# Kernel tuning notes

Hardware: AMD Instinct MI355X
Metric: run time of the kernel (lower is better)

## Reference

```python
import jax, jax.numpy as jnp
import numpy as np

B, L, D, R = 8, 2048, 512, 512  # batch, seq, feature, n_rules


def setup_inputs() -> dict:
    key = jax.random.key(0)
    ks = jax.random.split(key, 6)
    query = jax.random.normal(ks[0], (B, L, D), dtype=jnp.float32)
    # to_q: Linear(D, D)
    Wq = jax.random.normal(ks[1], (D, D), dtype=jnp.float32) / np.sqrt(D)
    bq = jnp.zeros((D,), dtype=jnp.float32)
    # to_c: Linear(L, R)
    Wc = jax.random.normal(ks[2], (R, L), dtype=jnp.float32) / np.sqrt(L)
    bc = jnp.zeros((R,), dtype=jnp.float32)
    # fuzzy rule params, torch.rand init (uniform [0,1)); widths kept away from 0
    centers = jax.random.uniform(ks[3], (R, D), dtype=jnp.float32)
    widths = jax.random.uniform(ks[4], (R, D), dtype=jnp.float32, minval=0.1, maxval=1.0)
    return {"query": query, "Wq": Wq, "bq": bq, "Wc": Wc, "bc": bc,
            "centers": centers, "widths": widths}


def reference(query, Wq, bq, Wc, bc, centers, widths):
    # q = to_q(query)  (projection=True)
    q = query @ Wq.T + bq  # (B, L, D)
    # z[b,l,r] = -0.5 * mean_d (|q - c| / w)^2 ; abs is a no-op under the square,
    # so expand (q - c)^2 / w^2 into three GEMM-friendly terms (exact same math).
    inv_w2 = 1.0 / (widths * widths)                      # (R, D)
    qq = (q * q) @ inv_w2.T                               # (B, L, R)
    qc = q @ (centers * inv_w2).T                         # (B, L, R)
    cc = jnp.sum(centers * centers * inv_w2, axis=-1)     # (R,)
    z = -(0.5 / D) * (qq - 2.0 * qc + cc)                 # (B, L, R)
    Fss = jax.nn.softmax(z, axis=-1)                      # (B, L, R); dropout p=0
    # conq = to_c applied along the L axis of query, yielding (B, R, D)
    conq = jnp.einsum('bld,rl->brd', query, Wc) + bc[None, :, None]
    return Fss @ conq                                     # (B, L, D)
```

## Files before the change

kernel.cpp:

```cpp
#include <hip/hip_runtime.h>
#include <hip/hip_bf16.h>

constexpr int Bb = 8, Ls = 2048, Dd = 512, Rr = 512;
constexpr int M1 = Bb * Ls;

typedef _Float16 h8v __attribute__((ext_vector_type(8)));
typedef _Float16 h4v __attribute__((ext_vector_type(4)));
typedef float f4v __attribute__((ext_vector_type(4)));

__device__ __forceinline__ void async_copy16(const void* g, void* l) {
  __builtin_amdgcn_global_load_lds((const __attribute__((address_space(1))) unsigned int*)g,
                                   (__attribute__((address_space(3))) unsigned int*)l, 16, 0, 0);
}

__device__ __forceinline__ void swizzle_xy(int& x, int& yy) {
  const int NX = gridDim.x;
  const int lin = ((int)blockIdx.z * (int)gridDim.y + (int)blockIdx.y) * NX + (int)blockIdx.x;
  const int xcd = lin & 7;
  const int w = lin >> 3;
  x = w % NX;
  yy = (w / NX) * 8 + xcd;
}

__global__ __launch_bounds__(256) void prep_all(
    const float* __restrict__ q, _Float16* __restrict__ qs, _Float16* __restrict__ qt,
    const float* __restrict__ Wq, _Float16* __restrict__ wq,
    const float* __restrict__ Wc, _Float16* __restrict__ wc,
    const float* __restrict__ centers, const float* __restrict__ widths,
    _Float16* __restrict__ iwh, _Float16* __restrict__ c2h, float* __restrict__ cc) {
  const int bid = blockIdx.x, tid = threadIdx.x;
  if (bid < 2048) {
    __shared__ float t[64][65];
    const int b = bid >> 8;
    const int l0 = ((bid >> 3) & 31) * 64;
    const int d0 = (bid & 7) * 64;
    const int r = tid >> 4, c4 = (tid & 15) * 4;
#pragma unroll
    for (int i = 0; i < 4; ++i) {
      const int l = r + i * 16;
      const float4 v = *(const float4*)&q[((long)b * Ls + l0 + l) * Dd + d0 + c4];
      t[l][c4] = v.x; t[l][c4 + 1] = v.y; t[l][c4 + 2] = v.z; t[l][c4 + 3] = v.w;
      h4v h = {(_Float16)v.x, (_Float16)v.y, (_Float16)v.z, (_Float16)v.w};
      *(h4v*)&qs[((long)b * Ls + l0 + l) * Dd + d0 + c4] = h;
    }
    __syncthreads();
#pragma unroll
    for (int i = 0; i < 4; ++i) {
      const int d = r + i * 16;
      h4v h = {(_Float16)t[c4][d], (_Float16)t[c4 + 1][d],
               (_Float16)t[c4 + 2][d], (_Float16)t[c4 + 3][d]};
      *(h4v*)&qt[((long)b * Dd + d0 + d) * Ls + l0 + c4] = h;
    }
  } else if (bid < 2304) {
    const int i = (bid - 2048) * 256 + tid;
    float4 v = *(const float4*)&Wq[(long)i * 4];
    h4v o = {(_Float16)v.x, (_Float16)v.y, (_Float16)v.z, (_Float16)v.w};
    *(h4v*)&wq[(long)i * 4] = o;
  } else if (bid < 3328) {
    const int i = (bid - 2304) * 256 + tid;
    float4 v = *(const float4*)&Wc[(long)i * 4];
    h4v o = {(_Float16)v.x, (_Float16)v.y, (_Float16)v.z, (_Float16)v.w};
    *(h4v*)&wc[(long)i * 4] = o;
  } else {
    const int wave = tid >> 6, lane = tid & 63;
    const int r = (bid - 3328) * 4 + wave;
    float s = 0.f;
#pragma unroll
    for (int j = 0; j < 8; ++j) {
      const int d = j * 64 + lane;
      const float c = centers[(long)r * Dd + d];
      const float w = widths[(long)r * Dd + d];
      const float iw = 1.0f / (w * w);
      iwh[(long)r * Dd + d] = (_Float16)iw;
      c2h[(long)r * Dd + d] = (_Float16)(-2.0f * c * iw);
      s += c * c * iw;
    }
#pragma unroll
    for (int o = 32; o > 0; o >>= 1) s += __shfl_xor(s, o, 64);
    if (lane == 0) cc[r] = s;
  }
}

template <int WM, int EPI>
__global__ __launch_bounds__(512, 4) void gemm_h(
    const _Float16* __restrict__ A, const _Float16* __restrict__ Bm,
    const float* __restrict__ bias, float* __restrict__ Cf,
    _Float16* __restrict__ Ch, int Kext, int ldA, int ldB, int ldC, int kstep,
    long sA, long sB, long sC) {
  constexpr int TM = WM * 32;
  __shared__ _Float16 As[2][TM * 32];
  __shared__ _Float16 Bs[2][128 * 32];
  int x, yy;
  swizzle_xy(x, yy);
  const int y = yy % (int)gridDim.y;
  const int zz = yy / (int)gridDim.y;
  const int n0 = x * 128;
  const int m0 = y * TM;
  const int kb = zz * kstep;
  const _Float16* Ab = A + (long)zz * sA;
  const _Float16* Bb = Bm + (long)zz * sB;

  const int tid = threadIdx.x;
  const int wave = tid >> 6, lane = tid & 63;
  const int wm = wave >> 2, wn = wave & 3;
  const int quad = lane >> 4, tr = lane & 15;
  const int lrow = lane >> 2;
  const int lcol = (lane & 3) * 8;

  f4v acc[WM][2];
#pragma unroll
  for (int i = 0; i < WM; ++i)
#pragma unroll
    for (int j = 0; j < 2; ++j) acc[i][j] = (f4v){0.f, 0.f, 0.f, 0.f};

  for (int k0 = 0; k0 < Kext; k0 += 64) {
    __syncthreads();
#pragma unroll
    for (int c = wave; c < TM / 16; c += 8) {
      const long g = (long)(m0 + c * 16 + lrow) * ldA + kb + k0 + lcol;
      async_copy16(Ab + g, &As[0][c * 512]);
      async_copy16(Ab + g + 32, &As[1][c * 512]);
    }
#pragma unroll
    for (int c = wave; c < 8; c += 8) {
      const long g = (long)(n0 + c * 16 + lrow) * ldB + kb + k0 + lcol;
      async_copy16(Bb + g, &Bs[0][c * 512]);
      async_copy16(Bb + g + 32, &Bs[1][c * 512]);
    }
    __syncthreads();

#pragma unroll
    for (int h = 0; h < 2; ++h) {
      h8v af[WM], bf[2];
#pragma unroll
      for (int i = 0; i < WM; ++i)
        af[i] = *(const h8v*)&As[h][(wm * (WM * 16) + i * 16 + tr) * 32 + quad * 8];
#pragma unroll
      for (int j = 0; j < 2; ++j)
        bf[j] = *(const h8v*)&Bs[h][(wn * 32 + j * 16 + tr) * 32 + quad * 8];
#pragma unroll
      for (int i = 0; i < WM; ++i)
#pragma unroll
        for (int j = 0; j < 2; ++j)
          acc[i][j] = __builtin_amdgcn_mfma_f32_16x16x32_f16(af[i], bf[j], acc[i][j], 0, 0, 0);
    }
  }

  float* Cfb = Cf ? Cf + (long)zz * sC : nullptr;
  _Float16* Chb = Ch ? Ch + (long)zz * sC : nullptr;
#pragma unroll
  for (int i = 0; i < WM; ++i)
#pragma unroll
    for (int j = 0; j < 2; ++j) {
      const int rbase = m0 + wm * (WM * 16) + i * 16 + quad * 4;
      const int cg = n0 + wn * 32 + j * 16 + tr;
#pragma unroll
      for (int r = 0; r < 4; ++r) {
        const float v = acc[i][j][r];
        const long row = rbase + r;
        if (EPI == 2) {
          Chb[row * (long)ldC + cg] = (_Float16)(v + bias[cg]);
        } else if (EPI == 3) {
          Cfb[row * (long)ldC + cg] = v;
        }
      }
    }
}

__global__ __launch_bounds__(512, 4) void zq_gemm(
    const _Float16* __restrict__ Q, const _Float16* __restrict__ Iw,
    const _Float16* __restrict__ C2, const float* __restrict__ cc,
    _Float16* __restrict__ Zh) {
  __shared__ _Float16 As[2][128 * 32];
  __shared__ _Float16 B1[2][128 * 32];
  __shared__ _Float16 B2[2][128 * 32];
  int x, yy;
  swizzle_xy(x, yy);
  const int n0 = x * 128;
  const int m0 = yy * 128;

  const int tid = threadIdx.x;
  const int wave = tid >> 6, lane = tid & 63;
  const int wm = wave >> 2, wn = wave & 3;
  const int quad = lane >> 4, tr = lane & 15;
  const int lrow = lane >> 2;
  const int lcol = (lane & 3) * 8;

  f4v acc[4][2];
#pragma unroll
  for (int i = 0; i < 4; ++i)
#pragma unroll
    for (int j = 0; j < 2; ++j) acc[i][j] = (f4v){0.f, 0.f, 0.f, 0.f};

  for (int k0 = 0; k0 < 512; k0 += 64) {
    __syncthreads();
    {
      const long ga = (long)(m0 + wave * 16 + lrow) * 512 + k0 + lcol;
      async_copy16(Q + ga, &As[0][wave * 512]);
      async_copy16(Q + ga + 32, &As[1][wave * 512]);
      const long gb = (long)(n0 + wave * 16 + lrow) * 512 + k0 + lcol;
      async_copy16(Iw + gb, &B1[0][wave * 512]);
      async_copy16(Iw + gb + 32, &B1[1][wave * 512]);
      async_copy16(C2 + gb, &B2[0][wave * 512]);
      async_copy16(C2 + gb + 32, &B2[1][wave * 512]);
    }
    __syncthreads();

#pragma unroll
    for (int h = 0; h < 2; ++h) {
      h8v af[4], af2[4], b1[2], b2[2];
#pragma unroll
      for (int i = 0; i < 4; ++i) {
        af[i] = *(const h8v*)&As[h][(wm * 64 + i * 16 + tr) * 32 + quad * 8];
        af2[i] = af[i] * af[i];
      }
#pragma unroll
      for (int j = 0; j < 2; ++j) {
        b1[j] = *(const h8v*)&B1[h][(wn * 32 + j * 16 + tr) * 32 + quad * 8];
        b2[j] = *(const h8v*)&B2[h][(wn * 32 + j * 16 + tr) * 32 + quad * 8];
      }
#pragma unroll
      for (int i = 0; i < 4; ++i)
#pragma unroll
        for (int j = 0; j < 2; ++j) {
          acc[i][j] = __builtin_amdgcn_mfma_f32_16x16x32_f16(af2[i], b1[j], acc[i][j], 0, 0, 0);
          acc[i][j] = __builtin_amdgcn_mfma_f32_16x16x32_f16(af[i], b2[j], acc[i][j], 0, 0, 0);
        }
    }
  }

  constexpr float zs = -0.0009765625f;
#pragma unroll
  for (int i = 0; i < 4; ++i)
#pragma unroll
    for (int j = 0; j < 2; ++j) {
      const int rbase = m0 + wm * 64 + i * 16 + quad * 4;
      const int cg = n0 + wn * 32 + j * 16 + tr;
      const float ccv = cc[cg];
#pragma unroll
      for (int r = 0; r < 4; ++r)
        Zh[(long)(rbase + r) * 512 + cg] = (_Float16)((acc[i][j][r] + ccv) * zs);
    }
}

__global__ __launch_bounds__(256) void softmax_h(const _Float16* __restrict__ Zh,
                                                 _Float16* __restrict__ F) {
  const int wave = threadIdx.x >> 6;
  const int lane = threadIdx.x & 63;
  const long row = (long)blockIdx.x * 4 + wave;
  h8v zv = *(const h8v*)&Zh[row * Rr + lane * 8];
  float v[8];
#pragma unroll
  for (int i = 0; i < 8; ++i) v[i] = (float)zv[i];
  float m = v[0];
#pragma unroll
  for (int i = 1; i < 8; ++i) m = fmaxf(m, v[i]);
#pragma unroll
  for (int s = 32; s > 0; s >>= 1) m = fmaxf(m, __shfl_xor(m, s, 64));
  float sum = 0.f;
#pragma unroll
  for (int i = 0; i < 8; ++i) {
    v[i] = __expf(v[i] - m);
    sum += v[i];
  }
#pragma unroll
  for (int s = 32; s > 0; s >>= 1) sum += __shfl_xor(sum, s, 64);
  const float inv = 1.0f / sum;
  h8v o;
#pragma unroll
  for (int i = 0; i < 8; ++i) o[i] = (_Float16)(v[i] * inv);
  *(h8v*)&F[row * Rr + lane * 8] = o;
}

extern "C" void kernel_launch(void* const* d_in, const int* in_sizes, int n_in,
                              void* d_out, int out_size, void* d_ws, size_t ws_size,
                              hipStream_t stream) {
  const float* query   = (const float*)d_in[0];
  const float* Wq      = (const float*)d_in[1];
  const float* bq      = (const float*)d_in[2];
  const float* Wc      = (const float*)d_in[3];
  const float* bc      = (const float*)d_in[4];
  const float* centers = (const float*)d_in[5];
  const float* widths  = (const float*)d_in[6];
  float* out = (float*)d_out;

  char* base = (char*)d_ws;
  auto alloc = [&](size_t bytes) {
    char* p = base;
    base += (bytes + 255) & ~(size_t)255;
    return p;
  };
  _Float16* qs  = (_Float16*)alloc((size_t)M1 * Dd * 2);
  _Float16* qt  = (_Float16*)alloc((size_t)M1 * Dd * 2);
  _Float16* q16 = (_Float16*)alloc((size_t)M1 * Dd * 2);
  _Float16* zh  = (_Float16*)alloc((size_t)M1 * Rr * 2);
  _Float16* fs  = (_Float16*)alloc((size_t)M1 * Rr * 2);
  _Float16* wq  = (_Float16*)alloc((size_t)Dd * Dd * 2);
  _Float16* wc  = (_Float16*)alloc((size_t)Rr * Ls * 2);
  _Float16* iwh = (_Float16*)alloc((size_t)Rr * Dd * 2);
  _Float16* c2h = (_Float16*)alloc((size_t)Rr * Dd * 2);
  float*    cc  = (float*)alloc((size_t)Rr * 4);
  _Float16* cq  = (_Float16*)alloc((size_t)Bb * Dd * Rr * 2);

  prep_all<<<3456, 256, 0, stream>>>(query, qs, qt, Wq, wq, Wc, wc,
                                     centers, widths, iwh, c2h, cc);

  gemm_h<4, 2><<<dim3(Dd / 128, M1 / 128, 1), 512, 0, stream>>>(
      qs, wq, bq, nullptr, q16, Dd, Dd, Dd, Dd, 0, 0, 0, 0);

  zq_gemm<<<dim3(Rr / 128, M1 / 128, 1), 512, 0, stream>>>(q16, iwh, c2h, cc, zh);

  softmax_h<<<M1 / 4, 256, 0, stream>>>(zh, fs);

  gemm_h<2, 2><<<dim3(Rr / 128, (Bb * Dd) / 64, 1), 512, 0, stream>>>(
      qt, wc, bc, nullptr, cq, Ls, Ls, Ls, Rr, 0, 0, 0, 0);

  gemm_h<4, 3><<<dim3(Dd / 128, Ls / 128, Bb), 512, 0, stream>>>(
      fs, cq, nullptr, out, nullptr, Rr, Rr, Rr, Dd, 0,
      (long)Ls * Rr, (long)Dd * Rr, (long)Ls * Dd);
}
```

Before: 186.6 us.

## Merge Q projection and conq GEMMs into one heterogeneous launch

Turns the GEMM kernel into a device body function with dynamic shared memory, then adds a combined kernel. In it, the first 256 blocks compute the conq projection (K=2048, WM=2) and the remaining 512 blocks compute the Q projection (WM=4). The two independent GEMMs now run concurrently in one launch, which fills the GPU better and removes one launch plus its tail. The long-K conq blocks are scheduled first so they start early. The XCD swizzle is now computed explicitly from a linear block index.

```diff
diff --git a/kernel.cpp b/kernel.cpp
--- a/kernel.cpp
+++ b/kernel.cpp
@@ -11,15 +11,6 @@
 __device__ __forceinline__ void async_copy16(const void* g, void* l) {
   __builtin_amdgcn_global_load_lds((const __attribute__((address_space(1))) unsigned int*)g,
                                    (__attribute__((address_space(3))) unsigned int*)l, 16, 0, 0);
-}
-
-__device__ __forceinline__ void swizzle_xy(int& x, int& yy) {
-  const int NX = gridDim.x;
-  const int lin = ((int)blockIdx.z * (int)gridDim.y + (int)blockIdx.y) * NX + (int)blockIdx.x;
-  const int xcd = lin & 7;
-  const int w = lin >> 3;
-  x = w % NX;
-  yy = (w / NX) * 8 + xcd;
 }
 
 __global__ __launch_bounds__(256) void prep_all(
@@ -82,23 +73,27 @@
 }
 
 template <int WM, int EPI>
-__global__ __launch_bounds__(512, 4) void gemm_h(
+__device__ __forceinline__ void gemm_body(
+    const int lin, const int NX, const int NY, _Float16* __restrict__ smem,
     const _Float16* __restrict__ A, const _Float16* __restrict__ Bm,
-    const float* __restrict__ bias, float* __restrict__ Cf,
-    _Float16* __restrict__ Ch, int Kext, int ldA, int ldB, int ldC, int kstep,
-    long sA, long sB, long sC) {
+    const float* __restrict__ bias, float* __restrict__ Cf, _Float16* __restrict__ Ch,
+    const int Kext, const int ldA, const int ldB, const int ldC, const int kstep,
+    const long sA, const long sB, const long sC) {
   constexpr int TM = WM * 32;
-  __shared__ _Float16 As[2][TM * 32];
-  __shared__ _Float16 Bs[2][128 * 32];
-  int x, yy;
-  swizzle_xy(x, yy);
-  const int y = yy % (int)gridDim.y;
-  const int zz = yy / (int)gridDim.y;
+  _Float16* As = smem;
+  _Float16* Bs = smem + TM * 64;
+
+  const int xcd = lin & 7;
+  const int wi = lin >> 3;
+  const int x = wi % NX;
+  const int yy = (wi / NX) * 8 + xcd;
+  const int y = yy % NY;
+  const int zz = yy / NY;
   const int n0 = x * 128;
   const int m0 = y * TM;
   const int kb = zz * kstep;
   const _Float16* Ab = A + (long)zz * sA;
-  const _Float16* Bb = Bm + (long)zz * sB;
+  const _Float16* Bbp = Bm + (long)zz * sB;
 
   const int tid = threadIdx.x;
   const int wave = tid >> 6, lane = tid & 63;
@@ -118,14 +113,14 @@
 #pragma unroll
     for (int c = wave; c < TM / 16; c += 8) {
       const long g = (long)(m0 + c * 16 + lrow) * ldA + kb + k0 + lcol;
-      async_copy16(Ab + g, &As[0][c * 512]);
-      async_copy16(Ab + g + 32, &As[1][c * 512]);
+      async_copy16(Ab + g, &As[c * 512]);
+      async_copy16(Ab + g + 32, &As[TM * 32 + c * 512]);
     }
 #pragma unroll
     for (int c = wave; c < 8; c += 8) {
       const long g = (long)(n0 + c * 16 + lrow) * ldB + kb + k0 + lcol;
-      async_copy16(Bb + g, &Bs[0][c * 512]);
-      async_copy16(Bb + g + 32, &Bs[1][c * 512]);
+      async_copy16(Bbp + g, &Bs[c * 512]);
+      async_copy16(Bbp + g + 32, &Bs[4096 + c * 512]);
     }
     __syncthreads();
 
@@ -134,10 +129,10 @@
       h8v af[WM], bf[2];
 #pragma unroll
       for (int i = 0; i < WM; ++i)
-        af[i] = *(const h8v*)&As[h][(wm * (WM * 16) + i * 16 + tr) * 32 + quad * 8];
+        af[i] = *(const h8v*)&As[h * (TM * 32) + (wm * (WM * 16) + i * 16 + tr) * 32 + quad * 8];
 #pragma unroll
       for (int j = 0; j < 2; ++j)
-        bf[j] = *(const h8v*)&Bs[h][(wn * 32 + j * 16 + tr) * 32 + quad * 8];
+        bf[j] = *(const h8v*)&Bs[h * 4096 + (wn * 32 + j * 16 + tr) * 32 + quad * 8];
 #pragma unroll
       for (int i = 0; i < WM; ++i)
 #pragma unroll
@@ -167,6 +162,35 @@
     }
 }
 
+template <int WM, int EPI>
+__global__ __launch_bounds__(512, 4) void gemm_h(
+    const _Float16* __restrict__ A, const _Float16* __restrict__ Bm,
+    const float* __restrict__ bias, float* __restrict__ Cf,
+    _Float16* __restrict__ Ch, int Kext, int ldA, int ldB, int ldC, int kstep,
+    long sA, long sB, long sC) {
+  extern __shared__ _Float16 smem[];
+  const int lin = ((int)blockIdx.z * (int)gridDim.y + (int)blockIdx.y) * (int)gridDim.x +
+                  (int)blockIdx.x;
+  gemm_body<WM, EPI>(lin, (int)gridDim.x, (int)gridDim.y, smem, A, Bm, bias, Cf, Ch,
+                     Kext, ldA, ldB, ldC, kstep, sA, sB, sC);
+}
+
+__global__ __launch_bounds__(512, 4) void qgemm_conq(
+    const _Float16* __restrict__ qs, const _Float16* __restrict__ wq,
+    const float* __restrict__ bq, _Float16* __restrict__ q16,
+    const _Float16* __restrict__ qt, const _Float16* __restrict__ wc,
+    const float* __restrict__ bc, _Float16* __restrict__ cq) {
+  extern __shared__ _Float16 smem[];
+  const int bid = (int)blockIdx.x;
+  if (bid < 256) {
+    gemm_body<2, 2>(bid, 4, 64, smem, qt, wc, bc, nullptr, cq,
+                    Ls, Ls, Ls, Rr, 0, 0, 0, 0);
+  } else {
+    gemm_body<4, 2>(bid - 256, 4, 128, smem, qs, wq, bq, nullptr, q16,
+                    Dd, Dd, Dd, Dd, 0, 0, 0, 0);
+  }
+}
+
 __global__ __launch_bounds__(512, 4) void zq_gemm(
     const _Float16* __restrict__ Q, const _Float16* __restrict__ Iw,
     const _Float16* __restrict__ C2, const float* __restrict__ cc,
@@ -174,8 +198,11 @@
   __shared__ _Float16 As[2][128 * 32];
   __shared__ _Float16 B1[2][128 * 32];
   __shared__ _Float16 B2[2][128 * 32];
-  int x, yy;
-  swizzle_xy(x, yy);
+  const int lin = (int)blockIdx.y * 4 + (int)blockIdx.x;
+  const int xcd = lin & 7;
+  const int wi = lin >> 3;
+  const int x = wi % 4;
+  const int yy = (wi / 4) * 8 + xcd;
   const int n0 = x * 128;
   const int m0 = yy * 128;
 
@@ -305,17 +332,13 @@
   prep_all<<<3456, 256, 0, stream>>>(query, qs, qt, Wq, wq, Wc, wc,
                                      centers, widths, iwh, c2h, cc);
 
-  gemm_h<4, 2><<<dim3(Dd / 128, M1 / 128, 1), 512, 0, stream>>>(
-      qs, wq, bq, nullptr, q16, Dd, Dd, Dd, Dd, 0, 0, 0, 0);
+  qgemm_conq<<<768, 512, 32768, stream>>>(qs, wq, bq, q16, qt, wc, bc, cq);
 
   zq_gemm<<<dim3(Rr / 128, M1 / 128, 1), 512, 0, stream>>>(q16, iwh, c2h, cc, zh);
 
   softmax_h<<<M1 / 4, 256, 0, stream>>>(zh, fs);
 
-  gemm_h<2, 2><<<dim3(Rr / 128, (Bb * Dd) / 64, 1), 512, 0, stream>>>(
-      qt, wc, bc, nullptr, cq, Ls, Ls, Ls, Rr, 0, 0, 0, 0);
-
-  gemm_h<4, 3><<<dim3(Dd / 128, Ls / 128, Bb), 512, 0, stream>>>(
+  gemm_h<4, 3><<<dim3(Dd / 128, Ls / 128, Bb), 512, 32768, stream>>>(
       fs, cq, nullptr, out, nullptr, Rr, Rr, Rr, Dd, 0,
       (long)Ls * Rr, (long)Dd * Rr, (long)Ls * Dd);
 }
```

Result: faster. 172.3 us (-7.6%).
